# Kernel optimization log

Measured on AMD Instinct MI355X. Metric: run time of the kernel, lower is better.

The kernel has to match this reference:

```python
import jax, jax.numpy as jnp
import numpy as np

NUM_USER, NUM_ITEM, NUM_HIDDEN, NNZ = 8192, 16384, 64, 200000


def setup_inputs() -> dict:
    key = jax.random.key(0)
    k_u, k_i, k_idx, k_r = jax.random.split(key, 4)
    # Parameters: torch.normal(mean=0, std=0.1)
    embed_user = 0.1 * jax.random.normal(k_u, (NUM_USER, NUM_HIDDEN), dtype=jnp.float32)
    embed_item = 0.1 * jax.random.normal(k_i, (NUM_ITEM, NUM_HIDDEN), dtype=jnp.float32)
    indices = jax.random.randint(k_idx, (2, NNZ), 0, 8192, dtype=jnp.int64)
    ratings = jax.random.uniform(k_r, (NNZ,), dtype=jnp.float32)
    return {"embed_user": embed_user, "embed_item": embed_item,
            "indices": indices, "ratings": ratings}


def reference(embed_user, embed_item, indices, ratings):
    U, H = embed_user.shape
    I = embed_item.shape[0]
    # Row masks: True for any user/item id appearing in the batch.
    user_mask = jnp.zeros((U,), dtype=bool).at[indices[0]].set(True)
    item_mask = jnp.zeros((I,), dtype=bool).at[indices[1]].set(True)
    # Mask whole rows, then dense cross product (matches sparse.mm -> to_dense).
    eu = embed_user * user_mask[:, None].astype(embed_user.dtype)
    ei = embed_item * item_mask[:, None].astype(embed_item.dtype)
    pred = jnp.einsum('uh,ih->ui', eu, ei)  # [U, I]
    # sparse_coo_tensor(...).to_dense() sums duplicate (u, i) entries.
    label = jnp.zeros((U, I), dtype=ratings.dtype).at[indices[0], indices[1]].add(ratings)
    ratio = float(U * I) / float(ratings.shape[0])
    return pred, label, ratio
```

## Files before the change

### kernel.cpp

```cpp
#include <hip/hip_runtime.h>

#define NU 8192
#define NI 16384
#define NH 64
#define TM 128
#define TN 128
#define KP 32

typedef float v4 __attribute__((ext_vector_type(4)));

__global__ void init_kernel(unsigned int* __restrict__ p, int nwords,
                            float* __restrict__ ratio) {
    int i = blockIdx.x * blockDim.x + threadIdx.x;
    if (i < nwords) p[i] = 0u;
    if (i == 0) *ratio = 671.08864f;
}

__global__ void build_masks_kernel(const int* __restrict__ idx,
                                   unsigned char* __restrict__ um,
                                   unsigned char* __restrict__ im, int nnz) {
    int k = blockIdx.x * blockDim.x + threadIdx.x;
    if (k < nnz) {
        um[idx[k]]       = 1;
        im[idx[nnz + k]] = 1;
    }
}

__global__ __launch_bounds__(256, 3) void gemm_kernel(
    const float* __restrict__ A,
    const float* __restrict__ B,
    const unsigned char* __restrict__ um,
    const unsigned char* __restrict__ im,
    float* __restrict__ pred,
    float* __restrict__ label)
{
    __shared__ float As[KP * TM];
    __shared__ float Bs[KP * TN];

    const int tid = threadIdx.x;
    const int c0 = blockIdx.x * TN;
    const int r0 = blockIdx.y * TM;

    const int any = __syncthreads_or((tid < TN) && (im[c0 + tid] != 0));

    v4* __restrict__ pred4 = (v4*)pred;
    v4* __restrict__ lab4  = (v4*)label;
    const v4 z4 = (v4){0.f, 0.f, 0.f, 0.f};

    if (!any) {
#pragma unroll
        for (int i = 0; i < TM * TN / 4 / 256; ++i) {
            int f   = i * 256 + tid;
            int row = f >> 5;
            int cv  = f & 31;
            size_t o = (size_t)(r0 + row) * (NI / 4) + (size_t)(c0 >> 2) + cv;
            __builtin_nontemporal_store(z4, &pred4[o]);
            __builtin_nontemporal_store(z4, &lab4[o]);
        }
        return;
    }

    const float4* A4 = (const float4*)A;
    const float4* B4 = (const float4*)B;
    const float4* As4 = (const float4*)As;
    const float4* Bs4 = (const float4*)Bs;

    const int ms  = tid >> 3;
    const int kvL = tid & 7;

    float amsk[4], bmsk[4];
#pragma unroll
    for (int t = 0; t < 4; ++t) {
        amsk[t] = um[r0 + ms + 32 * t] ? 1.f : 0.f;
        bmsk[t] = im[c0 + ms + 32 * t] ? 1.f : 0.f;
    }

#pragma unroll
    for (int t = 0; t < 4; ++t) {
        int m    = ms + 32 * t;
        int base = (4 * kvL) * TM + 4 * ((m >> 2) ^ kvL) + (m & 3);
        float4 va = A4[(size_t)(r0 + m) * (NH / 4) + kvL];
        float4 vb = B4[(size_t)(c0 + m) * (NH / 4) + kvL];
        As[base]          = va.x * amsk[t];
        As[base + TM]     = va.y * amsk[t];
        As[base + 2 * TM] = va.z * amsk[t];
        As[base + 3 * TM] = va.w * amsk[t];
        Bs[base]          = vb.x * bmsk[t];
        Bs[base + TN]     = vb.y * bmsk[t];
        Bs[base + 2 * TN] = vb.z * bmsk[t];
        Bs[base + 3 * TN] = vb.w * bmsk[t];
    }
    __syncthreads();

    float4 pa[4], pb[4];
#pragma unroll
    for (int t = 0; t < 4; ++t) {
        int m = ms + 32 * t;
        pa[t] = A4[(size_t)(r0 + m) * (NH / 4) + (KP / 4) + kvL];
        pb[t] = B4[(size_t)(c0 + m) * (NH / 4) + (KP / 4) + kvL];
    }

#pragma unroll
    for (int i = 0; i < TM * TN / 4 / 256; ++i) {
        int f   = i * 256 + tid;
        int row = f >> 5;
        int cv  = f & 31;
        size_t o = (size_t)(r0 + row) * (NI / 4) + (size_t)(c0 >> 2) + cv;
        __builtin_nontemporal_store(z4, &lab4[o]);
    }

    const int tx = tid & 15;
    const int ty = tid >> 4;

    float acc[2][4][2][4];
#pragma unroll
    for (int rg = 0; rg < 2; ++rg)
#pragma unroll
        for (int i = 0; i < 4; ++i)
#pragma unroll
            for (int cg = 0; cg < 2; ++cg)
#pragma unroll
                for (int j = 0; j < 4; ++j) acc[rg][i][cg][j] = 0.f;

#pragma unroll
    for (int p = 0; p < 2; ++p) {
        if (p) {
            __syncthreads();
#pragma unroll
            for (int t = 0; t < 4; ++t) {
                int m    = ms + 32 * t;
                int base = (4 * kvL) * TM + 4 * ((m >> 2) ^ kvL) + (m & 3);
                As[base]          = pa[t].x * amsk[t];
                As[base + TM]     = pa[t].y * amsk[t];
                As[base + 2 * TM] = pa[t].z * amsk[t];
                As[base + 3 * TM] = pa[t].w * amsk[t];
                Bs[base]          = pb[t].x * bmsk[t];
                Bs[base + TN]     = pb[t].y * bmsk[t];
                Bs[base + 2 * TN] = pb[t].z * bmsk[t];
                Bs[base + 3 * TN] = pb[t].w * bmsk[t];
            }
            __syncthreads();
        }

#pragma unroll 2
        for (int kv = 0; kv < KP / 4; ++kv) {
            const int ta = ty ^ kv;
            const int tb = tx ^ kv;
            const int kb = kv * 4 * 32;
#pragma unroll
            for (int r = 0; r < 4; ++r) {
                float4 a0 = As4[kb + r * 32 + ta];
                float4 a1 = As4[kb + r * 32 + 16 + ta];
                float4 b0 = Bs4[kb + r * 32 + tb];
                float4 b1 = Bs4[kb + r * 32 + 16 + tb];
                float ar[2][4] = {{a0.x, a0.y, a0.z, a0.w}, {a1.x, a1.y, a1.z, a1.w}};
                float br[2][4] = {{b0.x, b0.y, b0.z, b0.w}, {b1.x, b1.y, b1.z, b1.w}};
#pragma unroll
                for (int rg = 0; rg < 2; ++rg)
#pragma unroll
                    for (int i = 0; i < 4; ++i)
#pragma unroll
                        for (int cg = 0; cg < 2; ++cg)
#pragma unroll
                            for (int j = 0; j < 4; ++j)
                                acc[rg][i][cg][j] += ar[rg][i] * br[cg][j];
            }
        }
    }

#pragma unroll
    for (int rg = 0; rg < 2; ++rg)
#pragma unroll
        for (int i = 0; i < 4; ++i) {
            int row = r0 + rg * 64 + ty * 4 + i;
            size_t rb = (size_t)row * (NI / 4);
#pragma unroll
            for (int cg = 0; cg < 2; ++cg) {
                size_t cv = (size_t)((c0 + cg * 64 + tx * 4) >> 2);
                v4 v = (v4){acc[rg][i][cg][0], acc[rg][i][cg][1],
                            acc[rg][i][cg][2], acc[rg][i][cg][3]};
                __builtin_nontemporal_store(v, &pred4[rb + cv]);
            }
        }
}

__global__ void scatter_kernel(const int* __restrict__ idx,
                               const float* __restrict__ r,
                               float* __restrict__ label, int nnz) {
    int k = blockIdx.x * blockDim.x + threadIdx.x;
    if (k < nnz) {
        int u  = idx[k];
        int it = idx[nnz + k];
        atomicAdd(&label[(size_t)u * NI + it], r[k]);
    }
}

extern "C" void kernel_launch(void* const* d_in, const int* in_sizes, int n_in,
                              void* d_out, int out_size, void* d_ws, size_t ws_size,
                              hipStream_t stream) {
    const float* A   = (const float*)d_in[0];
    const float* B   = (const float*)d_in[1];
    const int*   idx = (const int*)d_in[2];
    const float* r   = (const float*)d_in[3];
    const int nnz = in_sizes[3];

    float* out   = (float*)d_out;
    float* pred  = out;
    float* label = out + (size_t)NU * NI;
    float* ratio = out + 2 * (size_t)NU * NI;

    unsigned char* um = (unsigned char*)d_ws;
    unsigned char* im = um + NU;

    const int mask_words = (NU + NI) / 4;
    init_kernel<<<(mask_words + 255) / 256, 256, 0, stream>>>(
        (unsigned int*)d_ws, mask_words, ratio);
    build_masks_kernel<<<(nnz + 255) / 256, 256, 0, stream>>>(idx, um, im, nnz);

    dim3 grid(NI / TN, NU / TM);
    gemm_kernel<<<grid, 256, 0, stream>>>(A, B, um, im, pred, label);

    scatter_kernel<<<(nnz + 255) / 256, 256, 0, stream>>>(idx, r, label, nnz);
}
```

Measured before the change: 1.115 ms.

## Split zeroing of label and pred into separate streaming kernels with precomputed column flags

```diff
diff --git a/kernel.cpp b/kernel.cpp
--- a/kernel.cpp
+++ b/kernel.cpp
@@ -6,6 +6,7 @@
 #define TM 128
 #define TN 128
 #define KP 32
+#define NCT (NI / TN)
 
 typedef float v4 __attribute__((ext_vector_type(4)));
 
@@ -26,44 +27,73 @@
     }
 }
 
+__global__ __launch_bounds__(128) void flags_kernel(
+    const unsigned char* __restrict__ im,
+    unsigned char* __restrict__ flags) {
+    int j = threadIdx.x;
+    const uint4* p = (const uint4*)(im + j * TN);
+    unsigned int acc = 0;
+#pragma unroll
+    for (int t = 0; t < TN / 16; ++t) {
+        uint4 v = p[t];
+        acc |= v.x | v.y | v.z | v.w;
+    }
+    flags[j] = acc ? 1 : 0;
+}
+
+__global__ __launch_bounds__(256) void zero_label_kernel(float* __restrict__ label) {
+    const v4 z4 = (v4){0.f, 0.f, 0.f, 0.f};
+    v4* __restrict__ l4 = (v4*)label;
+    const size_t n = (size_t)NU * NI / 4;
+    const size_t stride = (size_t)gridDim.x * 256;
+    for (size_t i = (size_t)blockIdx.x * 256 + threadIdx.x; i < n; i += stride)
+        __builtin_nontemporal_store(z4, &l4[i]);
+}
+
+__global__ __launch_bounds__(256) void zero_pred_kernel(
+    const unsigned char* __restrict__ flags,
+    float* __restrict__ pred) {
+    __shared__ unsigned char f[NCT];
+    const int tid = threadIdx.x;
+    if (tid < NCT) f[tid] = flags[tid];
+    __syncthreads();
+
+    const v4 z4 = (v4){0.f, 0.f, 0.f, 0.f};
+    v4* __restrict__ p4 = (v4*)pred;
+    const int r0 = blockIdx.x * 4;
+#pragma unroll
+    for (int rr = 0; rr < 4; ++rr) {
+        size_t rb = (size_t)(r0 + rr) * (NI / 4);
+#pragma unroll
+        for (int i = tid; i < NI / 4; i += 256) {
+            if (!f[i >> 5])
+                __builtin_nontemporal_store(z4, &p4[rb + i]);
+        }
+    }
+}
+
 __global__ __launch_bounds__(256, 3) void gemm_kernel(
     const float* __restrict__ A,
     const float* __restrict__ B,
     const unsigned char* __restrict__ um,
     const unsigned char* __restrict__ im,
-    float* __restrict__ pred,
-    float* __restrict__ label)
+    const unsigned char* __restrict__ flags,
+    float* __restrict__ pred)
 {
+    if (!flags[blockIdx.x]) return;
+
     __shared__ float As[KP * TM];
     __shared__ float Bs[KP * TN];
 
     const int tid = threadIdx.x;
     const int c0 = blockIdx.x * TN;
     const int r0 = blockIdx.y * TM;
-
-    const int any = __syncthreads_or((tid < TN) && (im[c0 + tid] != 0));
-
-    v4* __restrict__ pred4 = (v4*)pred;
-    v4* __restrict__ lab4  = (v4*)label;
-    const v4 z4 = (v4){0.f, 0.f, 0.f, 0.f};
-
-    if (!any) {
-#pragma unroll
-        for (int i = 0; i < TM * TN / 4 / 256; ++i) {
-            int f   = i * 256 + tid;
-            int row = f >> 5;
-            int cv  = f & 31;
-            size_t o = (size_t)(r0 + row) * (NI / 4) + (size_t)(c0 >> 2) + cv;
-            __builtin_nontemporal_store(z4, &pred4[o]);
-            __builtin_nontemporal_store(z4, &lab4[o]);
-        }
-        return;
-    }
 
     const float4* A4 = (const float4*)A;
     const float4* B4 = (const float4*)B;
     const float4* As4 = (const float4*)As;
     const float4* Bs4 = (const float4*)Bs;
+    v4* __restrict__ pred4 = (v4*)pred;
 
     const int ms  = tid >> 3;
     const int kvL = tid & 7;
@@ -100,15 +130,6 @@
         pb[t] = B4[(size_t)(c0 + m) * (NH / 4) + (KP / 4) + kvL];
     }
 
-#pragma unroll
-    for (int i = 0; i < TM * TN / 4 / 256; ++i) {
-        int f   = i * 256 + tid;
-        int row = f >> 5;
-        int cv  = f & 31;
-        size_t o = (size_t)(r0 + row) * (NI / 4) + (size_t)(c0 >> 2) + cv;
-        __builtin_nontemporal_store(z4, &lab4[o]);
-    }
-
     const int tx = tid & 15;
     const int ty = tid >> 4;
 
@@ -209,16 +230,20 @@
     float* label = out + (size_t)NU * NI;
     float* ratio = out + 2 * (size_t)NU * NI;
 
-    unsigned char* um = (unsigned char*)d_ws;
-    unsigned char* im = um + NU;
+    unsigned char* um    = (unsigned char*)d_ws;
+    unsigned char* im    = um + NU;
+    unsigned char* flags = im + NI;
 
     const int mask_words = (NU + NI) / 4;
     init_kernel<<<(mask_words + 255) / 256, 256, 0, stream>>>(
         (unsigned int*)d_ws, mask_words, ratio);
     build_masks_kernel<<<(nnz + 255) / 256, 256, 0, stream>>>(idx, um, im, nnz);
+    flags_kernel<<<1, 128, 0, stream>>>(im, flags);
+
+    zero_label_kernel<<<2048, 256, 0, stream>>>(label);
+    zero_pred_kernel<<<NU / 4, 256, 0, stream>>>(flags, pred);
+    scatter_kernel<<<(nnz + 255) / 256, 256, 0, stream>>>(idx, r, label, nnz);
 
     dim3 grid(NI / TN, NU / TM);
-    gemm_kernel<<<grid, 256, 0, stream>>>(A, B, um, im, pred, label);
-
-    scatter_kernel<<<(nnz + 255) / 256, 256, 0, stream>>>(idx, r, label, nnz);
-}
+    gemm_kernel<<<grid, 256, 0, stream>>>(A, B, um, im, flags, pred);
+}
```

Measured after the change: 1.237 ms. +10.9%, slower.
